# Kernel tuning notes

Measured on AMD Instinct MI355X. Metric: run time of the kernel, lower is better.

The kernel has to match this reference:

```python
import jax, jax.numpy as jnp
import numpy as np
from jax import lax

H = 2048          # hidden_size
NAH = 16          # num attn heads
AHD = H // NAH    # 128
NFH = 4           # num lact (fast-weight) heads
FHD = H // NFH    # 512 = d_in = d_out
DH = FHD          # d_h = d_in * inter_multi (1.0)
WIN = 1024        # sliding window
CHUNK = 512       # lact chunk size
B, S = 2, 2048
ROPE_BASE = 500000.0
EPS = 1e-6
BASE_LR_INV = 0.001 + float(np.log(-np.expm1(-0.001)))  # inv_softplus(1e-3)


def rms_norm(x, w):
    return x * lax.rsqrt(jnp.mean(x * x, axis=-1, keepdims=True) + EPS) * w


def silu(x):
    return x * jax.nn.sigmoid(x)


def silu_backprop(dy, x):
    sg = jax.nn.sigmoid(x)
    return dy * sg * (1.0 + x * (1.0 - sg))


def apply_rope(q, k):
    # q,k: [b,s,h,d]; non-interleaved (half-split) rotary, matching flash-attn RotaryEmbedding
    d = q.shape[-1]
    inv_freq = 1.0 / (ROPE_BASE ** (jnp.arange(0, d, 2, dtype=jnp.float32) / d))
    t = jnp.arange(q.shape[1], dtype=jnp.float32)
    freqs = jnp.outer(t, inv_freq)                       # [s, d/2]
    cos = jnp.cos(freqs)[None, :, None, :]
    sin = jnp.sin(freqs)[None, :, None, :]
    def rot(x):
        x1, x2 = jnp.split(x, 2, axis=-1)
        return jnp.concatenate([x1 * cos - x2 * sin, x2 * cos + x1 * sin], axis=-1)
    return rot(q), rot(k)


def sliding_window_attn(q, k, v):
    # [b,s,h,d]; causal sliding-window attention
    s = q.shape[1]
    scale = 1.0 / np.sqrt(q.shape[-1])
    i = jnp.arange(s)[:, None]
    j = jnp.arange(s)[None, :]
    mask = (j <= i) & (i - j < WIN)                      # [s,s]
    scores = jnp.einsum('bihd,bjhd->bhij', q, k) * scale
    scores = jnp.where(mask[None, None], scores, -jnp.inf)
    p = jax.nn.softmax(scores, axis=-1)
    return jnp.einsum('bhij,bjhd->bihd', p, v)


def setup_inputs() -> dict:
    key = jax.random.key(0)
    ks = jax.random.split(key, 10)
    def n(k, shape, scale):
        return jax.random.normal(k, shape, dtype=jnp.float32) * scale
    return {
        'hidden_states': n(ks[0], (B, S, H), 1.0),
        'attn_qkv_w': n(ks[1], (3 * H, H), 0.02),
        'attn_o_w': n(ks[2], (H, H), 0.02),
        'q_norm_w': jnp.ones((H,), jnp.float32),
        'k_norm_w': jnp.ones((H,), jnp.float32),
        'mlp_norm_w': jnp.ones((H,), jnp.float32),
        'mlp_qkv_w': n(ks[3], (3 * NFH * FHD, H), 0.02),
        'mlp_o_w': n(ks[4], (H, NFH * FHD), 0.02),
        'lr_w': n(ks[5], (3 * NFH, H), 0.02),
        'lr_b': jnp.zeros((3 * NFH,), jnp.float32),
        'w0': n(ks[6], (NFH, DH, FHD), 1.0 / np.sqrt(FHD)),
        'w1': n(ks[7], (NFH, FHD, DH), 1.0 / np.sqrt(DH)),
        'w2': n(ks[8], (NFH, DH, FHD), 1.0 / np.sqrt(FHD)),
        'ttt_norm_w': jnp.ones((FHD,), jnp.float32),
    }


def _forward(hidden_states, attn_qkv_w, attn_o_w, q_norm_w, k_norm_w, mlp_norm_w,
             mlp_qkv_w, mlp_o_w, lr_w, lr_b, w0, w1, w2, ttt_norm_w):
    b, s, _ = hidden_states.shape
    # ---- sliding window attention (token mixer) ----
    qkv = hidden_states @ attn_qkv_w.T
    q, k, v = jnp.split(qkv, 3, axis=-1)
    q = rms_norm(q, q_norm_w)
    k = rms_norm(k, k_norm_w)
    q = q.reshape(b, s, NAH, AHD)
    k = k.reshape(b, s, NAH, AHD)
    v = v.reshape(b, s, NAH, AHD)
    q, k = apply_rope(q, k)
    o = sliding_window_attn(q, k, v)
    attn_out = o.reshape(b, s, H) @ attn_o_w.T

    # ---- TTT-MLP SwiGLU fast-weight channel mixer after SWA ----
    x = rms_norm(attn_out, mlp_norm_w)
    fqkv = x @ mlp_qkv_w.T
    fq, fk, fv = jnp.split(fqkv, 3, axis=-1)
    fq, fk, fv = silu(fq), silu(fk), silu(fv)
    fq = fq.reshape(b, s, NFH, FHD)
    fk = fk.reshape(b, s, NFH, FHD)
    fv = fv.reshape(b, s, NFH, FHD)
    fq = fq / jnp.clip(jnp.linalg.norm(fq, axis=-1, keepdims=True), 1e-6)
    fk = fk / jnp.clip(jnp.linalg.norm(fk, axis=-1, keepdims=True), 1e-6)

    # per-token lrs (mamba parameterization: softplus(proj + inv_softplus(base_lr)))
    lr = jax.nn.softplus(x @ lr_w.T + lr_b + BASE_LR_INV)   # [b,s,3*NFH]
    l0, l1, l2 = jnp.split(lr, 3, axis=-1)                  # each [b,s,NFH]

    nc = s // CHUNK
    def chunkify(t):  # [b,s,h,d] -> [nc,b,h,c,d]
        return t.reshape(b, nc, CHUNK, t.shape[2], t.shape[3]).transpose(1, 0, 3, 2, 4)
    qs = chunkify(fq)
    ks_ = chunkify(fk)
    vs = chunkify(fv)
    l0s = chunkify(l0[..., None])
    l1s = chunkify(l1[..., None])
    l2s = chunkify(l2[..., None])

    w0b = jnp.broadcast_to(w0[None], (b,) + w0.shape)
    w1b = jnp.broadcast_to(w1[None], (b,) + w1.shape)
    w2b = jnp.broadcast_to(w2[None], (b,) + w2.shape)

    def step(carry, inp):
        cw0, cw1, cw2 = carry
        qc, kc, vc, lr0, lr1, lr2 = inp   # qc/kc/vc: [b,h,c,d]; lr*: [b,h,c,1]
        # apply current fast weights to queries of this chunk (apply-then-update)
        gq = jnp.einsum('bhed,bhcd->bhce', cw0, qc)
        hq = silu(gq) * jnp.einsum('bhed,bhcd->bhce', cw2, qc)
        oc = jnp.einsum('bhoe,bhce->bhco', cw1, hq)
        # update fast weights with this chunk's (k, v) under negative dot-product loss
        gk = jnp.einsum('bhed,bhcd->bhce', cw0, kc)      # gate pre-act
        hbm = jnp.einsum('bhed,bhcd->bhce', cw2, kc)     # hidden before mul
        hid = silu(gk) * hbm
        dhid = jnp.einsum('bhoe,bhco->bhce', cw1, vc)    # grad wrt hidden
        dhbm = dhid * silu(gk)
        dgate = dhid * hbm
        dgpre = silu_backprop(dgate, gk)
        nw1 = cw1 + jnp.einsum('bhco,bhce->bhoe', vc * lr1, hid)
        nw0 = cw0 + jnp.einsum('bhce,bhcd->bhed', dgpre, kc * lr0)
        nw2 = cw2 + jnp.einsum('bhce,bhcd->bhed', dhbm, kc * lr2)
        return (nw0, nw1, nw2), oc

    _, ocs = lax.scan(step, (w0b, w1b, w2b), (qs, ks_, vs, l0s, l1s, l2s))
    o_fw = ocs.transpose(1, 0, 3, 2, 4).reshape(b, s, NFH, FHD)
    o_fw = rms_norm(o_fw, ttt_norm_w)
    ttt_out = o_fw.reshape(b, s, NFH * FHD) @ mlp_o_w.T
    return attn_out + ttt_out


def reference(hidden_states, attn_qkv_w, attn_o_w, q_norm_w, k_norm_w, mlp_norm_w,
              mlp_qkv_w, mlp_o_w, lr_w, lr_b, w0, w1, w2, ttt_norm_w):
    return _forward(hidden_states, attn_qkv_w, attn_o_w, q_norm_w, k_norm_w, mlp_norm_w,
                    mlp_qkv_w, mlp_o_w, lr_w, lr_b, w0, w1, w2, ttt_norm_w)
```

## Files before the change

### kernel.cpp

```cpp
#include <hip/hip_runtime.h>
#include <cmath>

typedef unsigned short u16;
typedef unsigned int u32;
typedef short s16x8 __attribute__((ext_vector_type(8)));
typedef short s16x4 __attribute__((ext_vector_type(4)));
typedef float f32x4 __attribute__((ext_vector_type(4)));

#define DEV static __device__ __forceinline__

DEV float b2f(u16 h) { return __uint_as_float(((u32)h) << 16); }
DEV u16 f2b(float f) {
  u32 u = __float_as_uint(f);
  u = (u + 0x7FFFu + ((u >> 16) & 1u)) >> 16;
  return (u16)u;
}
DEV float siluf(float x) { return x / (1.f + __expf(-x)); }

DEV void gload16(const void* g, void* l) {
  __builtin_amdgcn_global_load_lds((const __attribute__((address_space(1))) void*)g,
                                   (__attribute__((address_space(3))) void*)l, 16, 0, 0);
}

DEV s16x8 lds_frag(const u16* buf, int row, int kg) {
  int lin = row * 64 + kg * 16;
  int adr = lin ^ (((row >> 1) & 3) << 4);
  return *(const s16x8*)((const char*)buf + adr);
}

template <int MODE>
__global__ __launch_bounds__(512, 1) void gemm_deep(const u16* __restrict__ A, const u16* __restrict__ B,
                                                    void* __restrict__ Cout, const float* __restrict__ Cin,
                                                    int ldc, int K, int gx) {
  __shared__ __align__(16) u16 Al[4][256 * 32];
  __shared__ __align__(16) u16 Bl[4][256 * 32];
  int tid = threadIdx.x, w = tid >> 6, l = tid & 63;
  int cpx = gx >> 3;
  int idx = blockIdx.x >> 3;
  int bx = (blockIdx.x & 7) * cpx + idx % cpx;
  int by = idx / cpx;
  const u16* Ab = A + (long)by * 256 * K;
  const u16* Bb = B + (long)bx * 256 * K;
  int wr = w >> 2, wc = w & 3;
  int fro = l & 15, kg = l >> 4;
  f32x4 acc[8][4] = {};
  int nk = K >> 5;

  auto stage = [&](int buf, int kt) {
    #pragma unroll
    for (int i = 0; i < 2; ++i) {
      int x = (tid + i * 512) * 16;
      int y = x ^ (((x >> 7) & 3) << 4);
      gload16(Ab + (long)(y >> 6) * K + kt * 32 + ((y & 63) >> 1), (char*)&Al[buf][0] + x);
    }
    #pragma unroll
    for (int i = 0; i < 2; ++i) {
      int x = (tid + i * 512) * 16;
      int y = x ^ (((x >> 7) & 3) << 4);
      gload16(Bb + (long)(y >> 6) * K + kt * 32 + ((y & 63) >> 1), (char*)&Bl[buf][0] + x);
    }
  };

  stage(0, 0);
  stage(1, 1);
  stage(2, 2);
  asm volatile("s_waitcnt vmcnt(8)" ::: "memory");
  __builtin_amdgcn_s_barrier();

  int cur = 0;
  for (int t = 0; t < nk; ++t) {
    const u16* Ac = &Al[cur][0];
    const u16* Bc = &Bl[cur][0];
    s16x8 af[8], bfr[4];
    #pragma unroll
    for (int m = 0; m < 8; ++m) af[m] = lds_frag(Ac, wr * 128 + m * 16 + fro, kg);
    #pragma unroll
    for (int n = 0; n < 4; ++n) bfr[n] = lds_frag(Bc, wc * 64 + n * 16 + fro, kg);
    if (t + 3 < nk) stage((cur + 3) & 3, t + 3);
    __builtin_amdgcn_s_setprio(1);
    #pragma unroll
    for (int m = 0; m < 8; ++m)
      #pragma unroll
      for (int n = 0; n < 4; ++n)
        acc[m][n] = __builtin_amdgcn_mfma_f32_16x16x32_bf16(af[m], bfr[n], acc[m][n], 0, 0, 0);
    __builtin_amdgcn_s_setprio(0);
    if (t + 3 < nk)      asm volatile("s_waitcnt vmcnt(8)" ::: "memory");
    else if (t + 2 < nk) asm volatile("s_waitcnt vmcnt(4)" ::: "memory");
    else if (t + 1 < nk) asm volatile("s_waitcnt vmcnt(0)" ::: "memory");
    __builtin_amdgcn_s_barrier();
    cur = (cur + 1) & 3;
  }

  long rbase = (long)by * 256 + wr * 128 + kg * 4;
  long cbase = (long)bx * 256 + wc * 64 + fro;
  #pragma unroll
  for (int m = 0; m < 8; ++m)
    #pragma unroll
    for (int n = 0; n < 4; ++n)
      #pragma unroll
      for (int j = 0; j < 4; ++j) {
        long r = rbase + m * 16 + j;
        long c = cbase + n * 16;
        float v = acc[m][n][j];
        if (MODE == 2) v += Cin[r * ldc + c];
        if (MODE == 0) ((u16*)Cout)[r * ldc + c] = f2b(v);
        else ((float*)Cout)[r * ldc + c] = v;
      }
}

template <int MODE>
__global__ __launch_bounds__(256, 3) void gemm128(const u16* __restrict__ A, const u16* __restrict__ B,
                                                  void* __restrict__ Cout, const float* __restrict__ Cin,
                                                  int ldc, int K, int gx) {
  __shared__ __align__(16) u16 Al[3][128 * 32];
  __shared__ __align__(16) u16 Bl[3][128 * 32];
  int tid = threadIdx.x, w = tid >> 6, l = tid & 63;
  int cpx = gx >> 3;
  int idx = blockIdx.x >> 3;
  int bx = (blockIdx.x & 7) * cpx + idx % cpx;
  int by = idx / cpx;
  const u16* Ab = A + (long)by * 128 * K;
  const u16* Bb = B + (long)bx * 128 * K;
  int wr = w >> 1, wc = w & 1;
  int fro = l & 15, kg = l >> 4;
  f32x4 acc[4][4] = {};
  int nk = K >> 5;

  auto stage = [&](int buf, int kt) {
    #pragma unroll
    for (int i = 0; i < 2; ++i) {
      int x = (tid + i * 256) * 16;
      int y = x ^ (((x >> 7) & 3) << 4);
      gload16(Ab + (long)(y >> 6) * K + kt * 32 + ((y & 63) >> 1), (char*)&Al[buf][0] + x);
      gload16(Bb + (long)(y >> 6) * K + kt * 32 + ((y & 63) >> 1), (char*)&Bl[buf][0] + x);
    }
  };

  stage(0, 0);
  stage(1, 1);
  asm volatile("s_waitcnt vmcnt(4)" ::: "memory");
  __builtin_amdgcn_s_barrier();

  int cur = 0;
  for (int t = 0; t < nk; ++t) {
    const u16* Ac = &Al[cur][0];
    const u16* Bc = &Bl[cur][0];
    s16x8 af[4], bfr[4];
    #pragma unroll
    for (int m = 0; m < 4; ++m) af[m] = lds_frag(Ac, wr * 64 + m * 16 + fro, kg);
    #pragma unroll
    for (int n = 0; n < 4; ++n) bfr[n] = lds_frag(Bc, wc * 64 + n * 16 + fro, kg);
    if (t + 2 < nk) {
      int nb = cur + 2; if (nb >= 3) nb -= 3;
      stage(nb, t + 2);
    }
    __builtin_amdgcn_s_setprio(1);
    #pragma unroll
    for (int m = 0; m < 4; ++m)
      #pragma unroll
      for (int n = 0; n < 4; ++n)
        acc[m][n] = __builtin_amdgcn_mfma_f32_16x16x32_bf16(af[m], bfr[n], acc[m][n], 0, 0, 0);
    __builtin_amdgcn_s_setprio(0);
    if (t + 2 < nk)      asm volatile("s_waitcnt vmcnt(4)" ::: "memory");
    else if (t + 1 < nk) asm volatile("s_waitcnt vmcnt(0)" ::: "memory");
    __builtin_amdgcn_s_barrier();
    if (++cur == 3) cur = 0;
  }

  long rbase = (long)by * 128 + wr * 64 + kg * 4;
  long cbase = (long)bx * 128 + wc * 64 + fro;
  #pragma unroll
  for (int m = 0; m < 4; ++m)
    #pragma unroll
// ... 17 lines not shown
  int lda, ldb, ldc, ldcb, ldct, K;
};
struct GemmBatch { GemmDesc d[5]; int nbh; };

__global__ __launch_bounds__(256, 3) void gemm_bt(GemmBatch gb) {
  int di = blockIdx.z / gb.nbh;
  int bh = blockIdx.z % gb.nbh;
  GemmDesc d = gb.d[di];
  __shared__ __align__(16) u16 As[3][4096];
  __shared__ __align__(16) u16 Bs[3][4096];
  int tid = threadIdx.x, w = tid >> 6, l = tid & 63;
  int b2 = bh >> 2, h2 = bh & 3;
  const u16* Ab = d.A + (long)b2 * d.sAb + (long)h2 * d.sAh + (long)blockIdx.y * 128 * d.lda;
  const u16* Bb = d.B + (long)b2 * d.sBb + (long)h2 * d.sBh + (long)blockIdx.x * 128 * d.ldb;
  f32x4 acc[4][4] = {};
  int nk = d.K >> 5;

  auto stage = [&](int buf, int kt) {
    #pragma unroll
    for (int i = 0; i < 2; ++i) {
      int x = (tid + i * 256) * 16;
      int y = x ^ (((x >> 7) & 3) << 4);
      gload16(Ab + (long)(y >> 6) * d.lda + kt * 32 + ((y & 63) >> 1), (char*)&As[buf][0] + x);
      gload16(Bb + (long)(y >> 6) * d.ldb + kt * 32 + ((y & 63) >> 1), (char*)&Bs[buf][0] + x);
    }
  };

  stage(0, 0);
  stage(1, 1);
  asm volatile("s_waitcnt vmcnt(4)" ::: "memory");
  __builtin_amdgcn_s_barrier();

  int wr = (w >> 1) * 64, wc = (w & 1) * 64;
  int fro = l & 15, kg = l >> 4;

  int cur = 0;
  for (int kt = 0; kt < nk; ++kt) {
    const u16* Ac = &As[cur][0];
    const u16* Bc = &Bs[cur][0];
    s16x8 af[4], bfr[4];
    #pragma unroll
    for (int m = 0; m < 4; ++m) af[m] = lds_frag(Ac, wr + m * 16 + fro, kg);
    #pragma unroll
    for (int n = 0; n < 4; ++n) bfr[n] = lds_frag(Bc, wc + n * 16 + fro, kg);
    if (kt + 2 < nk) {
      int nb = cur + 2; if (nb >= 3) nb -= 3;
      stage(nb, kt + 2);
    }
    __builtin_amdgcn_s_setprio(1);
    #pragma unroll
    for (int m = 0; m < 4; ++m)
      #pragma unroll
      for (int n = 0; n < 4; ++n)
        acc[m][n] = __builtin_amdgcn_mfma_f32_16x16x32_bf16(af[m], bfr[n], acc[m][n], 0, 0, 0);
    __builtin_amdgcn_s_setprio(0);
    if (kt + 2 < nk)      asm volatile("s_waitcnt vmcnt(4)" ::: "memory");
    else if (kt + 1 < nk) asm volatile("s_waitcnt vmcnt(0)" ::: "memory");
    __builtin_amdgcn_s_barrier();
    if (++cur == 3) cur = 0;
  }

  float* Cp = d.C ? d.C + (long)b2 * d.sCb_ + (long)h2 * d.sCh_ : nullptr;
  const float* Ci = d.Cin ? d.Cin + (long)b2 * d.sCb_ + (long)h2 * d.sCh_ : nullptr;
  u16* Cbp = d.Cb ? d.Cb + (long)b2 * d.sCbb + (long)h2 * d.sCbh : nullptr;
  u16* Ctp = d.CbT ? d.CbT + (long)b2 * d.sCtb + (long)h2 * d.sCth : nullptr;
  long rbase = (long)blockIdx.y * 128 + wr + kg * 4;
  long cbase = (long)blockIdx.x * 128 + wc + fro;
  #pragma unroll
  for (int m = 0; m < 4; ++m)
    #pragma unroll
    for (int n = 0; n < 4; ++n)
      #pragma unroll
      for (int j = 0; j < 4; ++j) {
        long r = rbase + m * 16 + j;
        long c = cbase + n * 16;
        float v = acc[m][n][j];
        if (Ci) v += Ci[r * d.ldc + c];
        if (Cp) Cp[r * d.ldc + c] = v;
        if (Cbp) Cbp[r * d.ldcb + c] = f2b(v);
        if (Ctp) Ctp[c * d.ldct + r] = f2b(v);
      }
}

__global__ __launch_bounds__(256) void convk(const float* __restrict__ in, u16* __restrict__ outp) {
  long i = ((long)blockIdx.x * 256 + threadIdx.x) * 4;
  float4 v = *(const float4*)(in + i);
  u16 o[4] __attribute__((aligned(8))) = {f2b(v.x), f2b(v.y), f2b(v.z), f2b(v.w)};
  *(s16x4*)&outp[i] = *(const s16x4*)o;
}

__global__ __launch_bounds__(256) void norm_rope_kernel(const u16* __restrict__ qkv,
    const float* __restrict__ qw, const float* __restrict__ kw,
    u16* __restrict__ qg, u16* __restrict__ kg, u16* __restrict__ vg) {
  __shared__ float qsh[2048], ksh[2048];
  __shared__ float red[2][4];
  int t = blockIdx.x, tid = threadIdx.x, w = tid >> 6, l = tid & 63;
  int s = t & 2047;
  const u16* row = qkv + (long)t * 6144;
  s16x8 vq = *(const s16x8*)&row[tid * 8];
  s16x8 vk = *(const s16x8*)&row[2048 + tid * 8];
  float sq = 0.f, sk = 0.f;
  #pragma unroll
  for (int i = 0; i < 8; ++i) {
    float a = b2f((u16)vq[i]); qsh[tid * 8 + i] = a; sq += a * a;
    float c = b2f((u16)vk[i]); ksh[tid * 8 + i] = c; sk += c * c;
  }
  *(s16x8*)&vg[(long)t * 2048 + tid * 8] = *(const s16x8*)&row[4096 + tid * 8];
  #pragma unroll
  for (int mk = 32; mk; mk >>= 1) { sq += __shfl_xor(sq, mk, 64); sk += __shfl_xor(sk, mk, 64); }
  if (l == 0) { red[0][w] = sq; red[1][w] = sk; }
  __syncthreads();
  float rq = rsqrtf((red[0][0] + red[0][1] + red[0][2] + red[0][3]) * (1.f / 2048.f) + 1e-6f);
  float rk = rsqrtf((red[1][0] + red[1][1] + red[1][2] + red[1][3]) * (1.f / 2048.f) + 1e-6f);
  const float lf = 13.122363377404329f / 64.f;
  #pragma unroll
  for (int ii = 0; ii < 4; ++ii) {
    int pid = tid + 256 * ii;
    int h = pid >> 6, dpos = pid & 63;
    float invf = expf(-(float)dpos * lf);
    float ang = (float)s * invf;
    float sn, cs;
    sincosf(ang, &sn, &cs);
    int i1 = h * 128 + dpos, i2 = i1 + 64;
    float q1 = qsh[i1] * rq * qw[i1], q2 = qsh[i2] * rq * qw[i2];
    qg[(long)t * 2048 + i1] = f2b(q1 * cs - q2 * sn);
    qg[(long)t * 2048 + i2] = f2b(q2 * cs + q1 * sn);
    float k1 = ksh[i1] * rk * kw[i1], k2v = ksh[i2] * rk * kw[i2];
    kg[(long)t * 2048 + i1] = f2b(k1 * cs - k2v * sn);
    kg[(long)t * 2048 + i2] = f2b(k2v * cs + k1 * sn);
  }
}

__global__ __launch_bounds__(256) void vtrans_kernel(const u16* __restrict__ v, u16* __restrict__ vT) {
  __shared__ u16 T[64][74];
  int tid = threadIdx.x;
  int bh = blockIdx.z, b = bh >> 4, h = bh & 15;
  int ts = blockIdx.x * 64, dg = blockIdx.y * 64;
  int r = tid >> 2, c0 = (tid & 3) * 16;
  const u16* src = v + ((long)b * 2048 + ts + r) * 2048 + h * 128 + dg + c0;
  *(s16x8*)&T[r][c0] = *(const s16x8*)src;
  *(s16x8*)&T[r][c0 + 8] = *(const s16x8*)(src + 8);
  __syncthreads();
  int d = tid >> 2, tg = (tid & 3) * 16;
  u16 a[16] __attribute__((aligned(16)));
  #pragma unroll
  for (int j = 0; j < 16; ++j) a[j] = T[tg + j][d];
  u16* dst = vT + ((long)bh * 128 + dg + d) * 2048 + ts + tg;
  *(s16x8*)dst = ((const s16x8*)a)[0];
  *(s16x8*)(dst + 8) = ((const s16x8*)a)[1];
}

__global__ __launch_bounds__(256, 2) void attn_kernel(const u16* __restrict__ qg, const u16* __restrict__ kg,
                                                      const u16* __restrict__ vT, u16* __restrict__ og) {
  __shared__ __align__(16) u16 Ks[64][136];
  __shared__ __align__(16) u16 Vt[128][72];
  __shared__ __align__(16) u16 Ps[4][32][72];
  int tid = threadIdx.x, w = tid >> 6, l = tid & 63;
  int h = blockIdx.y, b = blockIdx.z;
  int xs = ((blockIdx.x & 7) << 1) | (blockIdx.x >> 3);
  int qs = xs * 128;
  long tokb = (long)b * 2048;
  int fr = l & 15, fg = l >> 4;
  int wrow = qs + w * 32;

  s16x8 qf[2][4];
  #pragma unroll
  for (int rt = 0; rt < 2; ++rt)
    #pragma unroll
    for (int ks = 0; ks < 4; ++ks)
      qf[rt][ks] = *(const s16x8*)&qg[(tokb + wrow + rt * 16 + fr) * 2048 + h * 128 + ks * 32 + fg * 8];

  f32x4 oacc[2][8] = {};
  float mrun[2][4], lrun[2][4];
  #pragma unroll
  for (int rt = 0; rt < 2; ++rt)
    #pragma unroll
    for (int j = 0; j < 4; ++j) { mrun[rt][j] = -__builtin_inff(); lrun[rt][j] = 0.f; }

  int lo = qs - 1023;
  int t0 = lo > 0 ? (lo >> 6) : 0;
  int t1 = (qs + 127) >> 6;
  const float scale = 0.088388347648318447f;

  const u16* kbase = kg + tokb * 2048 + h * 128;
  const u16* vbase = vT + (long)(b * 16 + h) * 128 * 2048;

  s16x8 kreg[4], vreg[4];
  auto loadrg = [&](int kvs) {
    #pragma unroll
    for (int it = 0; it < 4; ++it) {
      int idx = it * 256 + tid;
      kreg[it] = *(const s16x8*)&kbase[(long)(kvs + (idx >> 4)) * 2048 + (idx & 15) * 8];
      vreg[it] = *(const s16x8*)&vbase[(long)(idx >> 3) * 2048 + kvs + (idx & 7) * 8];
    }
  };
  auto writelds = [&]() {
    #pragma unroll
    for (int it = 0; it < 4; ++it) {
      int idx = it * 256 + tid;
      *(s16x8*)&Ks[idx >> 4][(idx & 15) * 8] = kreg[it];
      *(s16x8*)&Vt[idx >> 3][(idx & 7) * 8] = vreg[it];
    }
  };

  loadrg(t0 << 6);
  writelds();
  __syncthreads();

  for (int kt = t0; kt <= t1; ++kt) {
    int kvs = kt << 6;
    if (kt < t1) loadrg((kt + 1) << 6);
    bool active = (kvs <= wrow + 31);
    if (active) {
      f32x4 st[2][4] = {};
      #pragma unroll
      for (int ct = 0; ct < 4; ++ct)
        #pragma unroll
        for (int ks = 0; ks < 4; ++ks) {
          s16x8 kf = *(const s16x8*)&Ks[ct * 16 + fr][ks * 32 + fg * 8];
          st[0][ct] = __builtin_amdgcn_mfma_f32_16x16x32_bf16(qf[0][ks], kf, st[0][ct], 0, 0, 0);
          st[1][ct] = __builtin_amdgcn_mfma_f32_16x16x32_bf16(qf[1][ks], kf, st[1][ct], 0, 0, 0);
        }
      bool needm = (kvs + 63 > wrow) || (kvs < wrow - 992);
      #pragma unroll
      for (int rt = 0; rt < 2; ++rt) {
        float mx[4];
        #pragma unroll
        for (int j = 0; j < 4; ++j) mx[j] = -__builtin_inff();
        #pragma unroll
        for (int ct = 0; ct < 4; ++ct)
          #pragma unroll
          for (int j = 0; j < 4; ++j) {
            float s = st[rt][ct][j] * scale;
            if (needm) {
              int r = wrow + rt * 16 + fg * 4 + j;
              int c = kvs + ct * 16 + fr;
              if (c > r || (r - c) >= 1024) s = -__builtin_inff();
            }
            st[rt][ct][j] = s;
            mx[j] = fmaxf(mx[j], s);
          }
        #pragma unroll
        for (int mk = 8; mk; mk >>= 1)
          #pragma unroll
          for (int j = 0; j < 4; ++j) mx[j] = fmaxf(mx[j], __shfl_xor(mx[j], mk, 64));
        float sc[4], nmu[4], rs[4];
        #pragma unroll
        for (int j = 0; j < 4; ++j) {
          float nm = fmaxf(mrun[rt][j], mx[j]);
          nmu[j] = (nm == -__builtin_inff()) ? 0.f : nm;
          sc[j] = __expf(mrun[rt][j] - nmu[j]);
          mrun[rt][j] = nm;
          rs[j] = 0.f;
        }
        #pragma unroll
        for (int ct = 0; ct < 4; ++ct)
          #pragma unroll
          for (int j = 0; j < 4; ++j) {
            float p = __expf(st[rt][ct][j] - nmu[j]);
            rs[j] += p;
            Ps[w][rt * 16 + fg * 4 + j][ct * 16 + fr] = f2b(p);
          }
        #pragma unroll
        for (int mk = 8; mk; mk >>= 1)
          #pragma unroll
          for (int j = 0; j < 4; ++j) rs[j] += __shfl_xor(rs[j], mk, 64);
        #pragma unroll
        for (int j = 0; j < 4; ++j) lrun[rt][j] = lrun[rt][j] * sc[j] + rs[j];
        #pragma unroll
        for (int dt = 0; dt < 8; ++dt)
          #pragma unroll
          for (int j = 0; j < 4; ++j) oacc[rt][dt][j] *= sc[j];
      }
      #pragma unroll
      for (int kst = 0; kst < 2; ++kst) {
        s16x8 pf0 = *(const s16x8*)&Ps[w][fr][kst * 32 + fg * 8];
        s16x8 pf1 = *(const s16x8*)&Ps[w][16 + fr][kst * 32 + fg * 8];
        #pragma unroll
        for (int dt = 0; dt < 8; ++dt) {
          s16x8 vf = *(const s16x8*)&Vt[dt * 16 + fr][kst * 32 + fg * 8];
          oacc[0][dt] = __builtin_amdgcn_mfma_f32_16x16x32_bf16(pf0, vf, oacc[0][dt], 0, 0, 0);
          oacc[1][dt] = __builtin_amdgcn_mfma_f32_16x16x32_bf16(pf1, vf, oacc[1][dt], 0, 0, 0);
        }
      }
    }
    __syncthreads();
    if (kt < t1) {
      writelds();
    }
    __syncthreads();
  }
  #pragma unroll
  for (int rt = 0; rt < 2; ++rt)
    #pragma unroll
    for (int j = 0; j < 4; ++j) {
      float inv = 1.f / lrun[rt][j];
      long rofs = (tokb + wrow + rt * 16 + fg * 4 + j) * 2048 + h * 128;
      #pragma unroll
      for (int dt = 0; dt < 8; ++dt)
        og[rofs + dt * 16 + fr] = f2b(oacc[rt][dt][j] * inv);
    }
}

__global__ __launch_bounds__(256) void rms_x_kernel(const float* __restrict__ src, const float* __restrict__ wgt,
                                                    u16* __restrict__ dst) {
  __shared__ float red[4];
  int t = blockIdx.x, tid = threadIdx.x, w = tid >> 6, l = tid & 63;
  const float* row = src + (long)t * 2048;
  float v[8] __attribute__((aligned(16)));
  ((float4*)v)[0] = *(const float4*)&row[tid * 8];
  ((float4*)v)[1] = *(const float4*)&row[tid * 8 + 4];
  float ss = 0.f;
  #pragma unroll
  for (int i = 0; i < 8; ++i) ss += v[i] * v[i];
  #pragma unroll
  for (int mk = 32; mk; mk >>= 1) ss += __shfl_xor(ss, mk, 64);
  if (l == 0) red[w] = ss;
  __syncthreads();
  float r = rsqrtf((red[0] + red[1] + red[2] + red[3]) * (1.f / 2048.f) + 1e-6f);
  #pragma unroll
  for (int i = 0; i < 8; ++i) dst[(long)t * 2048 + tid * 8 + i] = f2b(v[i] * r * wgt[tid * 8 + i]);
}

__global__ __launch_bounds__(256) void lr_kernel(const u16* __restrict__ xb, const float* __restrict__ lrw,
                                                 const float* __restrict__ lrbias, float* __restrict__ lrout,
                                                 float base) {
  __shared__ float red[4][12];
  int t = blockIdx.x, tid = threadIdx.x, w = tid >> 6, l = tid & 63;
  float xv[8];
  s16x8 rv = *(const s16x8*)&xb[(long)t * 2048 + tid * 8];
  #pragma unroll
  for (int i = 0; i < 8; ++i) xv[i] = b2f((u16)rv[i]);
  float acc[12];
  #pragma unroll
  for (int j = 0; j < 12; ++j) {
    const float4* w4 = (const float4*)(lrw + j * 2048 + tid * 8);
    float4 a = w4[0], bq = w4[1];
    acc[j] = xv[0] * a.x + xv[1] * a.y + xv[2] * a.z + xv[3] * a.w +
             xv[4] * bq.x + xv[5] * bq.y + xv[6] * bq.z + xv[7] * bq.w;
  }
  #pragma unroll
  for (int j = 0; j < 12; ++j)
    #pragma unroll
    for (int mk = 32; mk; mk >>= 1) acc[j] += __shfl_xor(acc[j], mk, 64);
  if (l == 0) {
    #pragma unroll
    for (int j = 0; j < 12; ++j) red[w][j] = acc[j];
  }
  __syncthreads();
  if (tid < 12) {
    float s_ = red[0][tid] + red[1][tid] + red[2][tid] + red[3][tid] + lrbias[tid] + base;
    lrout[(long)t * 12 + tid] = (s_ > 20.f) ? s_ : log1pf(__expf(s_));
  }
}

__global__ __launch_bounds__(256) void silu_norm_kernel(const u16* __restrict__ fqkv,
    u16* __restrict__ fqo, u16* __restrict__ fko, u16* __restrict__ fvo) {
  int t = blockIdx.x, tid = threadIdx.x, w = tid >> 6, l = tid & 63;
  const u16* row = fqkv + (long)t * 6144;
  {
    s16x8 rv = *(const s16x8*)&row[w * 512 + l * 8];
    float x[8]; float ss = 0.f;
    #pragma unroll
    for (int i = 0; i < 8; ++i) { x[i] = siluf(b2f((u16)rv[i])); ss += x[i] * x[i]; }
    #pragma unroll
    for (int mk = 32; mk; mk >>= 1) ss += __shfl_xor(ss, mk, 64);
    float sc = 1.f / fmaxf(sqrtf(ss), 1e-6f);
    #pragma unroll
    for (int i = 0; i < 8; ++i) fqo[(long)t * 2048 + w * 512 + l * 8 + i] = f2b(x[i] * sc);
  }
  {
    s16x8 rv = *(const s16x8*)&row[2048 + w * 512 + l * 8];
    float x[8]; float ss = 0.f;
    #pragma unroll
    for (int i = 0; i < 8; ++i) { x[i] = siluf(b2f((u16)rv[i])); ss += x[i] * x[i]; }
    #pragma unroll
    for (int mk = 32; mk; mk >>= 1) ss += __shfl_xor(ss, mk, 64);
    float sc = 1.f / fmaxf(sqrtf(ss), 1e-6f);
    #pragma unroll
    for (int i = 0; i < 8; ++i) fko[(long)t * 2048 + w * 512 + l * 8 + i] = f2b(x[i] * sc);
  }
  {
    s16x8 rv = *(const s16x8*)&row[4096 + tid * 8];
    #pragma unroll
// ... 100 lines not shown
    s16x8 va = *(const s16x8*)&fv[goff];
    s16x8 vb8 = *(const s16x8*)&fv[goff + 8];
    #pragma unroll
    for (int i = 0; i < 8; ++i) {
      float kv1 = b2f((u16)ka[i]), kv2 = b2f((u16)kb8[i]);
      float vv1 = b2f((u16)va[i]), vv2 = b2f((u16)vb8[i]);
      T0[r][c0 + i] = f2b(kv1 * l0);      T0[r][c0 + 8 + i] = f2b(kv2 * l0);
      T1[r][c0 + i] = f2b(kv1 * l2);      T1[r][c0 + 8 + i] = f2b(kv2 * l2);
      T2[r][c0 + i] = f2b(vv1 * l1);      T2[r][c0 + 8 + i] = f2b(vv2 * l1);
    }
  }
  __syncthreads();
  {
    u16 a0[16] __attribute__((aligned(16))), a1[16] __attribute__((aligned(16))), a2[16] __attribute__((aligned(16)));
    #pragma unroll
    for (int i = 0; i < 16; ++i) { a0[i] = T0[c0 + i][r]; a1[i] = T1[c0 + i][r]; a2[i] = T2[c0 + i][r]; }
    *(s16x8*)&k0T[obase] = ((const s16x8*)a0)[0];  *(s16x8*)&k0T[obase + 8] = ((const s16x8*)a0)[1];
    *(s16x8*)&k2T[obase] = ((const s16x8*)a1)[0];  *(s16x8*)&k2T[obase + 8] = ((const s16x8*)a1)[1];
    *(s16x8*)&v1T[obase] = ((const s16x8*)a2)[0];  *(s16x8*)&v1T[obase + 8] = ((const s16x8*)a2)[1];
  }
}

__global__ __launch_bounds__(256) void ttt_norm_kernel(const u16* __restrict__ src, const float* __restrict__ wgt,
                                                       u16* __restrict__ dst) {
  int t = blockIdx.x, tid = threadIdx.x, w = tid >> 6, l = tid & 63;
  long off = (long)t * 2048 + w * 512 + l * 8;
  s16x8 rv = *(const s16x8*)&src[off];
  float x[8];
  float ss = 0.f;
  #pragma unroll
  for (int i = 0; i < 8; ++i) { x[i] = b2f((u16)rv[i]); ss += x[i] * x[i]; }
  #pragma unroll
  for (int mk = 32; mk; mk >>= 1) ss += __shfl_xor(ss, mk, 64);
  float r = rsqrtf(ss * (1.f / 512.f) + 1e-6f);
  #pragma unroll
  for (int i = 0; i < 8; ++i) dst[off + i] = f2b(x[i] * r * wgt[l * 8 + i]);
}

extern "C" void kernel_launch(void* const* d_in, const int* in_sizes, int n_in,
                              void* d_out, int out_size, void* d_ws, size_t ws_size,
                              hipStream_t stream) {
  const float* hidden     = (const float*)d_in[0];
  const float* attn_qkv_w = (const float*)d_in[1];
  const float* attn_o_w   = (const float*)d_in[2];
  const float* q_norm_w   = (const float*)d_in[3];
  const float* k_norm_w   = (const float*)d_in[4];
  const float* mlp_norm_w = (const float*)d_in[5];
  const float* mlp_qkv_w  = (const float*)d_in[6];
  const float* mlp_o_w    = (const float*)d_in[7];
  const float* lr_w       = (const float*)d_in[8];
  const float* lr_bias    = (const float*)d_in[9];
  const float* w0in       = (const float*)d_in[10];
  const float* w1in       = (const float*)d_in[11];
  const float* w2in       = (const float*)d_in[12];
  const float* ttt_w      = (const float*)d_in[13];
  float* out = (float*)d_out;

  char* ws = (char*)d_ws;
  u16* hbf   = (u16*)(ws + 0);
  u16* wqb   = (u16*)(ws + 16777216);
  u16* wob   = (u16*)(ws + 41943040);
  char* big  = ws + 50331648;
  u16* qbuf  = (u16*)(ws + 121634816);
  u16* kbuf  = (u16*)(ws + 138412032);
  u16* vbuf  = (u16*)(ws + 155189248);
  u16* obuf  = (u16*)(ws + 171966464);
  float* lrb_ = (float*)(ws + 188743680);
  float* wbuf = (float*)(ws + 188940288);
  u16* wb16  = (u16*)(ws + 239271936);

  u16* qkvb = (u16*)big;
  u16* vTb  = (u16*)(big + 50331648);
  float* t5 = (float*)big;
  u16* hqb   = (u16*)(big + 41943040);
  u16* hidT  = (u16*)(big + 46137344);
  u16* dhbmT = (u16*)(big + 50331648);
  u16* dgpT  = (u16*)(big + 54525952);
  u16* k0T   = (u16*)(big + 58720256);
  u16* k2T   = (u16*)(big + 62914560);
  u16* v1T   = (u16*)(big + 67108864);
  u16* xb  = hbf;
  u16* ofw = hbf;

  convk<<<8192, 256, 0, stream>>>(hidden, hbf);
  convk<<<12288, 256, 0, stream>>>(attn_qkv_w, wqb);
  convk<<<4096, 256, 0, stream>>>(attn_o_w, wob);

  gemm_deep<0><<<384, 512, 0, stream>>>(hbf, wqb, qkvb, nullptr, 6144, 2048, 24);
  norm_rope_kernel<<<4096, 256, 0, stream>>>(qkvb, q_norm_w, k_norm_w, qbuf, kbuf, vbuf);
  vtrans_kernel<<<dim3(32, 2, 32), 256, 0, stream>>>(vbuf, vTb);
  attn_kernel<<<dim3(16, 16, 2), 256, 0, stream>>>(qbuf, kbuf, vTb, obuf);
  gemm128<1><<<512, 256, 0, stream>>>(obuf, wob, out, nullptr, 2048, 2048, 16);
  rms_x_kernel<<<4096, 256, 0, stream>>>(out, mlp_norm_w, xb);
  convk<<<12288, 256, 0, stream>>>(mlp_qkv_w, wqb);
  convk<<<4096, 256, 0, stream>>>(mlp_o_w, wob);
  float base_lr_inv = 0.001f + logf(-expm1f(-0.001f));
  lr_kernel<<<4096, 256, 0, stream>>>(xb, lr_w, lr_bias, lrb_, base_lr_inv);
  gemm_deep<0><<<384, 512, 0, stream>>>(xb, wqb, qkvb, nullptr, 6144, 2048, 24);
  silu_norm_kernel<<<4096, 256, 0, stream>>>(qkvb, qbuf, kbuf, vbuf);
  winit_kernel<<<6144, 256, 0, stream>>>(w0in, w1in, w2in, wbuf, wb16);

  for (int ic = 0; ic < 4; ++ic) {
    {
      GemmBatch g{}; g.nbh = 8;
      const u16* Asrc[5] = {qbuf, qbuf, kbuf, kbuf, vbuf};
      long Bwhich[5] = {0, 2, 0, 2, 3};
      for (int i = 0; i < 5; ++i) {
        GemmDesc& dd = g.d[i];
        dd.A = Asrc[i] + (long)ic * 1048576; dd.sAb = 4194304; dd.sAh = 512; dd.lda = 2048;
        dd.B = wb16 + Bwhich[i] * 2097152;   dd.sBb = 1048576; dd.sBh = 262144; dd.ldb = 512;
        dd.C = t5 + (long)i * 2097152;       dd.sCb_ = 1048576; dd.sCh_ = 262144; dd.ldc = 512;
        dd.K = 512;
      }
      gemm_bt<<<dim3(4, 4, 40), 256, 0, stream>>>(g);
    }
    ttt_elem_kernel<<<dim3(64, 8), 256, 0, stream>>>(t5, hqb, hidT, dhbmT, dgpT,
                                                     kbuf, vbuf, lrb_, k0T, k2T, v1T, ic);
    {
      GemmBatch g{}; g.nbh = 8;
      float* wc_ = wbuf + (long)(ic & 1) * 6291456;
      float* wn_ = wbuf + (long)((ic & 1) ^ 1) * 6291456;
      {
        GemmDesc& dd = g.d[0];
        dd.A = hqb; dd.sAb = 1048576; dd.sAh = 262144; dd.lda = 512;
        dd.B = wb16 + 2097152; dd.sBb = 1048576; dd.sBh = 262144; dd.ldb = 512;
        dd.Cb = ofw + (long)ic * 1048576; dd.sCbb = 4194304; dd.sCbh = 512; dd.ldcb = 2048;
        dd.K = 512;
      }
      const u16* A3[3] = {dgpT, v1T, dhbmT};
      const u16* B3[3] = {k0T, hidT, k2T};
      for (int i = 0; i < 3; ++i) {
        GemmDesc& dd = g.d[1 + i];
        dd.A = A3[i]; dd.sAb = 1048576; dd.sAh = 262144; dd.lda = 512;
        dd.B = B3[i]; dd.sBb = 1048576; dd.sBh = 262144; dd.ldb = 512;
        dd.Cin = wc_ + (long)i * 2097152; dd.C = wn_ + (long)i * 2097152;
        dd.sCb_ = 1048576; dd.sCh_ = 262144; dd.ldc = 512;
        dd.Cb = wb16 + (long)i * 2097152; dd.sCbb = 1048576; dd.sCbh = 262144; dd.ldcb = 512;
        if (i == 1) { dd.CbT = wb16 + 3L * 2097152; dd.sCtb = 1048576; dd.sCth = 262144; dd.ldct = 512; }
        dd.K = 512;
      }
      gemm_bt<<<dim3(4, 4, 32), 256, 0, stream>>>(g);
    }
  }
  ttt_norm_kernel<<<4096, 256, 0, stream>>>(ofw, ttt_w, obuf);
  gemm128<2><<<512, 256, 0, stream>>>(obuf, wob, out, out, 2048, 2048, 16);
  (void)in_sizes; (void)n_in; (void)out_size; (void)ws_size;
}
```

Before: 908.5 us.

## Restructure deep GEMM into eight-phase half-tile pipeline with interleaved loads

Replaces the 4-stage K=32 pipelined QKV GEMM with a double-buffered K=64 tile split into four half-tiles, each loaded separately. Each K step now runs four phases that interleave LDS fragment reads, one half-tile global prefetch, barriers and MFMA bursts. This is meant to overlap global-to-LDS traffic and LDS reads with matrix math more finely and to cut the fragment registers held at once. In exchange it adds many more barriers per K step, and the waitcnt bookkeeping is intricate.

New measurement: 918.5 us. No clear change (+1.1%).

```diff
diff --git a/kernel.cpp b/kernel.cpp
--- a/kernel.cpp
+++ b/kernel.cpp
@@ -29,11 +29,11 @@
 }
 
 template <int MODE>
-__global__ __launch_bounds__(512, 1) void gemm_deep(const u16* __restrict__ A, const u16* __restrict__ B,
-                                                    void* __restrict__ Cout, const float* __restrict__ Cin,
-                                                    int ldc, int K, int gx) {
-  __shared__ __align__(16) u16 Al[4][256 * 32];
-  __shared__ __align__(16) u16 Bl[4][256 * 32];
+__global__ __launch_bounds__(512, 1) void gemm8p(const u16* __restrict__ A, const u16* __restrict__ B,
+                                                 void* __restrict__ Cout, const float* __restrict__ Cin,
+                                                 int ldc, int K, int gx) {
+  __shared__ __align__(16) u16 Ah[2][2][8192];
+  __shared__ __align__(16) u16 Bh[2][2][8192];
   int tid = threadIdx.x, w = tid >> 6, l = tid & 63;
   int cpx = gx >> 3;
   int idx = blockIdx.x >> 3;
@@ -44,51 +44,107 @@
   int wr = w >> 2, wc = w & 3;
   int fro = l & 15, kg = l >> 4;
   f32x4 acc[8][4] = {};
-  int nk = K >> 5;
-
-  auto stage = [&](int buf, int kt) {
+  int nk = K >> 6;
+  int nht = nk << 2;
+
+  auto stage_ht = [&](int h) {
+    int tile = h >> 2, which = h & 3, db = tile & 1;
+    const u16* src = (which & 1) ? Bb : Ab;
+    u16* dst = (which & 1) ? &Bh[db][which >> 1][0] : &Ah[db][which >> 1][0];
+    int kcol = tile * 64 + (which >> 1) * 32;
     #pragma unroll
     for (int i = 0; i < 2; ++i) {
       int x = (tid + i * 512) * 16;
       int y = x ^ (((x >> 7) & 3) << 4);
-      gload16(Ab + (long)(y >> 6) * K + kt * 32 + ((y & 63) >> 1), (char*)&Al[buf][0] + x);
-    }
-    #pragma unroll
-    for (int i = 0; i < 2; ++i) {
-      int x = (tid + i * 512) * 16;
-      int y = x ^ (((x >> 7) & 3) << 4);
-      gload16(Bb + (long)(y >> 6) * K + kt * 32 + ((y & 63) >> 1), (char*)&Bl[buf][0] + x);
+      gload16(src + (long)(y >> 6) * K + kcol + ((y & 63) >> 1), (char*)dst + x);
     }
   };
 
-  stage(0, 0);
-  stage(1, 1);
-  stage(2, 2);
-  asm volatile("s_waitcnt vmcnt(8)" ::: "memory");
+  stage_ht(0); stage_ht(1); stage_ht(2); stage_ht(3);
+  asm volatile("s_waitcnt vmcnt(4)" ::: "memory");
+  stage_ht(4); stage_ht(5); stage_ht(6);
+  asm volatile("s_waitcnt vmcnt(6)" ::: "memory");
   __builtin_amdgcn_s_barrier();
 
-  int cur = 0;
+  int hnext = 7;
+  int arow = wr * 128 + fro, brow = wc * 64 + fro;
   for (int t = 0; t < nk; ++t) {
-    const u16* Ac = &Al[cur][0];
-    const u16* Bc = &Bl[cur][0];
-    s16x8 af[8], bfr[4];
-    #pragma unroll
-    for (int m = 0; m < 8; ++m) af[m] = lds_frag(Ac, wr * 128 + m * 16 + fro, kg);
-    #pragma unroll
-    for (int n = 0; n < 4; ++n) bfr[n] = lds_frag(Bc, wc * 64 + n * 16 + fro, kg);
-    if (t + 3 < nk) stage((cur + 3) & 3, t + 3);
+    int db = t & 1;
+    const u16 *A0 = &Ah[db][0][0], *A1 = &Ah[db][1][0];
+    const u16 *B0 = &Bh[db][0][0], *B1 = &Bh[db][1][0];
+    s16x8 af[4], bf[4];
+    #pragma unroll
+    for (int m = 0; m < 4; ++m) af[m] = lds_frag(A0, arow + m * 16, kg);
+    #pragma unroll
+    for (int n = 0; n < 4; ++n) bf[n] = lds_frag(B0, brow + n * 16, kg);
+    if (hnext < nht) stage_ht(hnext);
+    ++hnext;
+    __builtin_amdgcn_s_barrier();
+    asm volatile("s_waitcnt lgkmcnt(0)" ::: "memory");
+    __builtin_amdgcn_sched_barrier(0);
     __builtin_amdgcn_s_setprio(1);
     #pragma unroll
-    for (int m = 0; m < 8; ++m)
+    for (int m = 0; m < 4; ++m)
       #pragma unroll
       for (int n = 0; n < 4; ++n)
-        acc[m][n] = __builtin_amdgcn_mfma_f32_16x16x32_bf16(af[m], bfr[n], acc[m][n], 0, 0, 0);
+        acc[m][n] = __builtin_amdgcn_mfma_f32_16x16x32_bf16(af[m], bf[n], acc[m][n], 0, 0, 0);
     __builtin_amdgcn_s_setprio(0);
-    if (t + 3 < nk)      asm volatile("s_waitcnt vmcnt(8)" ::: "memory");
-    else if (t + 2 < nk) asm volatile("s_waitcnt vmcnt(4)" ::: "memory");
-    else if (t + 1 < nk) asm volatile("s_waitcnt vmcnt(0)" ::: "memory");
-    __builtin_amdgcn_s_barrier();
-    cur = (cur + 1) & 3;
+    __builtin_amdgcn_s_barrier();
+    #pragma unroll
+    for (int m = 0; m < 4; ++m) af[m] = lds_frag(A0, arow + (4 + m) * 16, kg);
+    if (hnext < nht) stage_ht(hnext);
+    ++hnext;
+    __builtin_amdgcn_s_barrier();
+    asm volatile("s_waitcnt lgkmcnt(0)" ::: "memory");
+    __builtin_amdgcn_sched_barrier(0);
+    __builtin_amdgcn_s_setprio(1);
+    #pragma unroll
+    for (int m = 0; m < 4; ++m)
+      #pragma unroll
+      for (int n = 0; n < 4; ++n)
+        acc[4 + m][n] = __builtin_amdgcn_mfma_f32_16x16x32_bf16(af[m], bf[n], acc[4 + m][n], 0, 0, 0);
+    __builtin_amdgcn_s_setprio(0);
+    __builtin_amdgcn_s_barrier();
+    #pragma unroll
+    for (int m = 0; m < 4; ++m) af[m] = lds_frag(A1, arow + m * 16, kg);
+    #pragma unroll
+    for (int n = 0; n < 4; ++n) bf[n] = lds_frag(B1, brow + n * 16, kg);
+    if (hnext < nht) stage_ht(hnext);
+    ++hnext;
+    __builtin_amdgcn_s_barrier();
+    asm volatile("s_waitcnt lgkmcnt(0)" ::: "memory");
+    __builtin_amdgcn_sched_barrier(0);
+    __builtin_amdgcn_s_setprio(1);
+    #pragma unroll
+    for (int m = 0; m < 4; ++m)
+      #pragma unroll
+      for (int n = 0; n < 4; ++n)
+        acc[m][n] = __builtin_amdgcn_mfma_f32_16x16x32_bf16(af[m], bf[n], acc[m][n], 0, 0, 0);
+    __builtin_amdgcn_s_setprio(0);
+    __builtin_amdgcn_s_barrier();
+    #pragma unroll
+    for (int m = 0; m < 4; ++m) af[m] = lds_frag(A1, arow + (4 + m) * 16, kg);
+    if (hnext < nht) stage_ht(hnext);
+    ++hnext;
+    __builtin_amdgcn_s_barrier();
+    asm volatile("s_waitcnt lgkmcnt(0)" ::: "memory");
+    __builtin_amdgcn_sched_barrier(0);
+    __builtin_amdgcn_s_setprio(1);
+    #pragma unroll
+    for (int m = 0; m < 4; ++m)
+      #pragma unroll
+      for (int n = 0; n < 4; ++n)
+        acc[4 + m][n] = __builtin_amdgcn_mfma_f32_16x16x32_bf16(af[m], bf[n], acc[4 + m][n], 0, 0, 0);
+    __builtin_amdgcn_s_setprio(0);
+    if (t + 1 < nk) {
+      int iss = hnext < nht ? hnext : nht;
+      int rem = iss - 4 * (t + 2);
+      if (rem >= 3)      asm volatile("s_waitcnt vmcnt(6)" ::: "memory");
+      else if (rem == 2) asm volatile("s_waitcnt vmcnt(4)" ::: "memory");
+      else if (rem == 1) asm volatile("s_waitcnt vmcnt(2)" ::: "memory");
+      else               asm volatile("s_waitcnt vmcnt(0)" ::: "memory");
+    }
+    __builtin_amdgcn_s_barrier();
   }
 
   long rbase = (long)by * 256 + wr * 128 + kg * 4;
@@ -760,7 +816,7 @@
   convk<<<12288, 256, 0, stream>>>(attn_qkv_w, wqb);
   convk<<<4096, 256, 0, stream>>>(attn_o_w, wob);
 
-  gemm_deep<0><<<384, 512, 0, stream>>>(hbf, wqb, qkvb, nullptr, 6144, 2048, 24);
+  gemm8p<0><<<384, 512, 0, stream>>>(hbf, wqb, qkvb, nullptr, 6144, 2048, 24);
   norm_rope_kernel<<<4096, 256, 0, stream>>>(qkvb, q_norm_w, k_norm_w, qbuf, kbuf, vbuf);
   vtrans_kernel<<<dim3(32, 2, 32), 256, 0, stream>>>(vbuf, vTb);
   attn_kernel<<<dim3(16, 16, 2), 256, 0, stream>>>(qbuf, kbuf, vTb, obuf);
@@ -770,7 +826,7 @@
   convk<<<4096, 256, 0, stream>>>(mlp_o_w, wob);
   float base_lr_inv = 0.001f + logf(-expm1f(-0.001f));
   lr_kernel<<<4096, 256, 0, stream>>>(xb, lr_w, lr_bias, lrb_, base_lr_inv);
-  gemm_deep<0><<<384, 512, 0, stream>>>(xb, wqb, qkvb, nullptr, 6144, 2048, 24);
+  gemm8p<0><<<384, 512, 0, stream>>>(xb, wqb, qkvb, nullptr, 6144, 2048, 24);
   silu_norm_kernel<<<4096, 256, 0, stream>>>(qkvb, qbuf, kbuf, vbuf);
   winit_kernel<<<6144, 256, 0, stream>>>(w0in, w1in, w2in, wbuf, wb16);
 
```

## Halve attention query tile to 64 rows and merge fp32-to-bf16 conversion launches

Applied to the files above, without the earlier changes.

The attention kernel now gives each block 64 query rows (16 per wave) instead of 128, doubling the grid to 1024 blocks with a remapped block order and raising launch bounds to 3 blocks per CU. This aims to improve occupancy and load balance over the causal sliding window, but each K/V tile is now reused by fewer query rows, so K/V loads grow. Separately, the fp32-to-bf16 weight and input conversions are merged into one multi-source kernel launch per phase to cut launch overhead.

Result: no change. 904.5 us (-0.4%).

```diff
diff --git a/kernel.cpp b/kernel.cpp
--- a/kernel.cpp
+++ b/kernel.cpp
@@ -272,11 +272,17 @@
       }
 }
 
-__global__ __launch_bounds__(256) void convk(const float* __restrict__ in, u16* __restrict__ outp) {
+__global__ __launch_bounds__(256) void convk3(const float* __restrict__ s0, u16* __restrict__ d0, long n0,
+                                              const float* __restrict__ s1, u16* __restrict__ d1, long n1,
+                                              const float* __restrict__ s2, u16* __restrict__ d2) {
   long i = ((long)blockIdx.x * 256 + threadIdx.x) * 4;
-  float4 v = *(const float4*)(in + i);
+  const float* s; u16* d;
+  if (i < n0) { s = s0; d = d0; }
+  else if (i < n0 + n1) { s = s1 - n0; d = d1 - n0; }
+  else { s = s2 - n0 - n1; d = d2 - n0 - n1; }
+  float4 v = *(const float4*)(s + i);
   u16 o[4] __attribute__((aligned(8))) = {f2b(v.x), f2b(v.y), f2b(v.z), f2b(v.w)};
-  *(s16x4*)&outp[i] = *(const s16x4*)o;
+  *(s16x4*)&d[i] = *(const s16x4*)o;
 }
 
 __global__ __launch_bounds__(256) void norm_rope_kernel(const u16* __restrict__ qkv,
@@ -340,36 +346,34 @@
   *(s16x8*)(dst + 8) = ((const s16x8*)a)[1];
 }
 
-__global__ __launch_bounds__(256, 2) void attn_kernel(const u16* __restrict__ qg, const u16* __restrict__ kg,
+__global__ __launch_bounds__(256, 3) void attn_kernel(const u16* __restrict__ qg, const u16* __restrict__ kg,
                                                       const u16* __restrict__ vT, u16* __restrict__ og) {
   __shared__ __align__(16) u16 Ks[64][136];
   __shared__ __align__(16) u16 Vt[128][72];
-  __shared__ __align__(16) u16 Ps[4][32][72];
+  __shared__ __align__(16) u16 Ps[4][16][72];
   int tid = threadIdx.x, w = tid >> 6, l = tid & 63;
-  int h = blockIdx.y, b = blockIdx.z;
-  int xs = ((blockIdx.x & 7) << 1) | (blockIdx.x >> 3);
-  int qs = xs * 128;
+  int lid = blockIdx.x + 32 * (blockIdx.y + 16 * blockIdx.z);
+  int nid = ((lid & 7) << 7) + (lid >> 3);
+  int bh = nid >> 5;
+  int h = bh & 15, b = bh >> 4;
+  int qs = (nid & 31) * 64;
   long tokb = (long)b * 2048;
   int fr = l & 15, fg = l >> 4;
-  int wrow = qs + w * 32;
-
-  s16x8 qf[2][4];
-  #pragma unroll
-  for (int rt = 0; rt < 2; ++rt)
-    #pragma unroll
-    for (int ks = 0; ks < 4; ++ks)
-      qf[rt][ks] = *(const s16x8*)&qg[(tokb + wrow + rt * 16 + fr) * 2048 + h * 128 + ks * 32 + fg * 8];
-
-  f32x4 oacc[2][8] = {};
-  float mrun[2][4], lrun[2][4];
-  #pragma unroll
-  for (int rt = 0; rt < 2; ++rt)
-    #pragma unroll
-    for (int j = 0; j < 4; ++j) { mrun[rt][j] = -__builtin_inff(); lrun[rt][j] = 0.f; }
+  int wrow = qs + w * 16;
+
+  s16x8 qf[4];
+  #pragma unroll
+  for (int ks = 0; ks < 4; ++ks)
+    qf[ks] = *(const s16x8*)&qg[(tokb + wrow + fr) * 2048 + h * 128 + ks * 32 + fg * 8];
+
+  f32x4 oacc[8] = {};
+  float mrun[4], lrun[4];
+  #pragma unroll
+  for (int j = 0; j < 4; ++j) { mrun[j] = -__builtin_inff(); lrun[j] = 0.f; }
 
   int lo = qs - 1023;
   int t0 = lo > 0 ? (lo >> 6) : 0;
-  int t1 = (qs + 127) >> 6;
+  int t1 = (qs + 63) >> 6;
   const float scale = 0.088388347648318447f;
 
   const u16* kbase = kg + tokb * 2048 + h * 128;
@@ -400,77 +404,71 @@
   for (int kt = t0; kt <= t1; ++kt) {
     int kvs = kt << 6;
     if (kt < t1) loadrg((kt + 1) << 6);
-    bool active = (kvs <= wrow + 31);
+    bool active = (kvs <= wrow + 15);
     if (active) {
-      f32x4 st[2][4] = {};
+      f32x4 st[4] = {};
       #pragma unroll
       for (int ct = 0; ct < 4; ++ct)
         #pragma unroll
         for (int ks = 0; ks < 4; ++ks) {
           s16x8 kf = *(const s16x8*)&Ks[ct * 16 + fr][ks * 32 + fg * 8];
-          st[0][ct] = __builtin_amdgcn_mfma_f32_16x16x32_bf16(qf[0][ks], kf, st[0][ct], 0, 0, 0);
-          st[1][ct] = __builtin_amdgcn_mfma_f32_16x16x32_bf16(qf[1][ks], kf, st[1][ct], 0, 0, 0);
+          st[ct] = __builtin_amdgcn_mfma_f32_16x16x32_bf16(qf[ks], kf, st[ct], 0, 0, 0);
         }
-      bool needm = (kvs + 63 > wrow) || (kvs < wrow - 992);
-      #pragma unroll
-      for (int rt = 0; rt < 2; ++rt) {
-        float mx[4];
-        #pragma unroll
-        for (int j = 0; j < 4; ++j) mx[j] = -__builtin_inff();
-        #pragma unroll
-        for (int ct = 0; ct < 4; ++ct)
-          #pragma unroll
-          for (int j = 0; j < 4; ++j) {
-            float s = st[rt][ct][j] * scale;
-            if (needm) {
-              int r = wrow + rt * 16 + fg * 4 + j;
-              int c = kvs + ct * 16 + fr;
-              if (c > r || (r - c) >= 1024) s = -__builtin_inff();
-            }
-            st[rt][ct][j] = s;
-            mx[j] = fmaxf(mx[j], s);
-          }
-        #pragma unroll
-        for (int mk = 8; mk; mk >>= 1)
-          #pragma unroll
-          for (int j = 0; j < 4; ++j) mx[j] = fmaxf(mx[j], __shfl_xor(mx[j], mk, 64));
-        float sc[4], nmu[4], rs[4];
+      bool needm = (kvs + 63 > wrow) || (kvs < wrow - 1008);
+      float mx[4];
+      #pragma unroll
+      for (int j = 0; j < 4; ++j) mx[j] = -__builtin_inff();
+      #pragma unroll
+      for (int ct = 0; ct < 4; ++ct)
         #pragma unroll
         for (int j = 0; j < 4; ++j) {
-          float nm = fmaxf(mrun[rt][j], mx[j]);
-          nmu[j] = (nm == -__builtin_inff()) ? 0.f : nm;
-          sc[j] = __expf(mrun[rt][j] - nmu[j]);
-          mrun[rt][j] = nm;
-          rs[j] = 0.f;
+          float s = st[ct][j] * scale;
+          if (needm) {
+            int r = wrow + fg * 4 + j;
+            int c = kvs + ct * 16 + fr;
+            if (c > r || (r - c) >= 1024) s = -__builtin_inff();
+          }
+          st[ct][j] = s;
+          mx[j] = fmaxf(mx[j], s);
         }
+      #pragma unroll
+      for (int mk = 8; mk; mk >>= 1)
         #pragma unroll
-        for (int ct = 0; ct < 4; ++ct)
-          #pragma unroll
-          for (int j = 0; j < 4; ++j) {
-            float p = __expf(st[rt][ct][j] - nmu[j]);
-            rs[j] += p;
-            Ps[w][rt * 16 + fg * 4 + j][ct * 16 + fr] = f2b(p);
-          }
+        for (int j = 0; j < 4; ++j) mx[j] = fmaxf(mx[j], __shfl_xor(mx[j], mk, 64));
+      float sc[4], nmu[4], rs[4];
+      #pragma unroll
+      for (int j = 0; j < 4; ++j) {
+        float nm = fmaxf(mrun[j], mx[j]);
+        nmu[j] = (nm == -__builtin_inff()) ? 0.f : nm;
+        sc[j] = __expf(mrun[j] - nmu[j]);
+        mrun[j] = nm;
+        rs[j] = 0.f;
+      }
+      #pragma unroll
+      for (int ct = 0; ct < 4; ++ct)
         #pragma unroll
-        for (int mk = 8; mk; mk >>= 1)
-          #pragma unroll
-          for (int j = 0; j < 4; ++j) rs[j] += __shfl_xor(rs[j], mk, 64);
+        for (int j = 0; j < 4; ++j) {
+          float p = __expf(st[ct][j] - nmu[j]);
+          rs[j] += p;
+          Ps[w][fg * 4 + j][ct * 16 + fr] = f2b(p);
+        }
+      #pragma unroll
+      for (int mk = 8; mk; mk >>= 1)
         #pragma unroll
-        for (int j = 0; j < 4; ++j) lrun[rt][j] = lrun[rt][j] * sc[j] + rs[j];
+        for (int j = 0; j < 4; ++j) rs[j] += __shfl_xor(rs[j], mk, 64);
+      #pragma unroll
+      for (int j = 0; j < 4; ++j) lrun[j] = lrun[j] * sc[j] + rs[j];
+      #pragma unroll
+      for (int dt = 0; dt < 8; ++dt)
         #pragma unroll
-        for (int dt = 0; dt < 8; ++dt)
-          #pragma unroll
-          for (int j = 0; j < 4; ++j) oacc[rt][dt][j] *= sc[j];
-      }
+        for (int j = 0; j < 4; ++j) oacc[dt][j] *= sc[j];
       #pragma unroll
       for (int kst = 0; kst < 2; ++kst) {
-        s16x8 pf0 = *(const s16x8*)&Ps[w][fr][kst * 32 + fg * 8];
-        s16x8 pf1 = *(const s16x8*)&Ps[w][16 + fr][kst * 32 + fg * 8];
+        s16x8 pf = *(const s16x8*)&Ps[w][fr][kst * 32 + fg * 8];
         #pragma unroll
         for (int dt = 0; dt < 8; ++dt) {
           s16x8 vf = *(const s16x8*)&Vt[dt * 16 + fr][kst * 32 + fg * 8];
-          oacc[0][dt] = __builtin_amdgcn_mfma_f32_16x16x32_bf16(pf0, vf, oacc[0][dt], 0, 0, 0);
-          oacc[1][dt] = __builtin_amdgcn_mfma_f32_16x16x32_bf16(pf1, vf, oacc[1][dt], 0, 0, 0);
+          oacc[dt] = __builtin_amdgcn_mfma_f32_16x16x32_bf16(pf, vf, oacc[dt], 0, 0, 0);
         }
       }
     }
@@ -481,15 +479,13 @@
     __syncthreads();
   }
   #pragma unroll
-  for (int rt = 0; rt < 2; ++rt)
-    #pragma unroll
-    for (int j = 0; j < 4; ++j) {
-      float inv = 1.f / lrun[rt][j];
-      long rofs = (tokb + wrow + rt * 16 + fg * 4 + j) * 2048 + h * 128;
-      #pragma unroll
-      for (int dt = 0; dt < 8; ++dt)
-        og[rofs + dt * 16 + fr] = f2b(oacc[rt][dt][j] * inv);
-    }
+  for (int j = 0; j < 4; ++j) {
+    float inv = 1.f / lrun[j];
+    long rofs = (tokb + wrow + fg * 4 + j) * 2048 + h * 128;
+    #pragma unroll
+    for (int dt = 0; dt < 8; ++dt)
+      og[rofs + dt * 16 + fr] = f2b(oacc[dt][j] * inv);
+  }
 }
 
 __global__ __launch_bounds__(256) void rms_x_kernel(const float* __restrict__ src, const float* __restrict__ wgt,
@@ -756,18 +752,18 @@
   u16* xb  = hbf;
   u16* ofw = hbf;
 
-  convk<<<8192, 256, 0, stream>>>(hidden, hbf);
-  convk<<<12288, 256, 0, stream>>>(attn_qkv_w, wqb);
-  convk<<<4096, 256, 0, stream>>>(attn_o_w, wob);
-
+  convk3<<<24576, 256, 0, stream>>>(hidden, hbf, 8388608L,
+                                    attn_qkv_w, wqb, 12582912L,
+                                    attn_o_w, wob);
   gemm_deep<0><<<384, 512, 0, stream>>>(hbf, wqb, qkvb, nullptr, 6144, 2048, 24);
   norm_rope_kernel<<<4096, 256, 0, stream>>>(qkvb, q_norm_w, k_norm_w, qbuf, kbuf, vbuf);
   vtrans_kernel<<<dim3(32, 2, 32), 256, 0, stream>>>(vbuf, vTb);
-  attn_kernel<<<dim3(16, 16, 2), 256, 0, stream>>>(qbuf, kbuf, vTb, obuf);
+  attn_kernel<<<dim3(32, 16, 2), 256, 0, stream>>>(qbuf, kbuf, vTb, obuf);
   gemm128<1><<<512, 256, 0, stream>>>(obuf, wob, out, nullptr, 2048, 2048, 16);
   rms_x_kernel<<<4096, 256, 0, stream>>>(out, mlp_norm_w, xb);
-  convk<<<12288, 256, 0, stream>>>(mlp_qkv_w, wqb);
-  convk<<<4096, 256, 0, stream>>>(mlp_o_w, wob);
+  convk3<<<16384, 256, 0, stream>>>(mlp_qkv_w, wqb, 12582912L,
+                                    mlp_o_w, wob, 4194304L,
+                                    mlp_o_w, wob);
   float base_lr_inv = 0.001f + logf(-expm1f(-0.001f));
   lr_kernel<<<4096, 256, 0, stream>>>(xb, lr_w, lr_bias, lrb_, base_lr_inv);
   gemm_deep<0><<<384, 512, 0, stream>>>(xb, wqb, qkvb, nullptr, 6144, 2048, 24);
```
